# Kernel tuning notes

Measured on AMD Instinct MI355X. Metric: run time of the kernel, lower is better.

The kernel has to match this reference:

```python
import jax, jax.numpy as jnp
import numpy as np

LAMBDA = 0.01  # sparsity_threshold
SCALE = 0.02
NUM_BLOCKS = 4


def setup_inputs() -> dict:
    key = jax.random.key(0)
    k1, k2, k3, k4, k5 = jax.random.split(key, 5)
    B, N, C = 8, 4096, 512
    bs = C // NUM_BLOCKS
    return {
        "x": jax.random.normal(k1, (B, N, C), dtype=jnp.float32),
        "w1": jax.random.normal(k2, (2, NUM_BLOCKS, bs, bs), dtype=jnp.float32) * SCALE,
        "w2": jax.random.normal(k3, (2, NUM_BLOCKS, bs, bs), dtype=jnp.float32) * SCALE,
        "b1": jax.random.normal(k4, (2, NUM_BLOCKS, bs), dtype=jnp.float32) * SCALE,
        "b2": jax.random.normal(k5, (2, NUM_BLOCKS, bs), dtype=jnp.float32) * SCALE,
        "H": 64,
        "W": 64,
    }


def _softshrink(v):
    return jnp.where(v > LAMBDA, v - LAMBDA, jnp.where(v < -LAMBDA, v + LAMBDA, jnp.zeros((), v.dtype)))


def reference(x, w1, w2, b1, b2, H, W):
    B, N, C = x.shape
    bs = C // NUM_BLOCKS
    xb = x.reshape(B, N, NUM_BLOCKS, bs)
    # FFT over (token, block) axes, ortho norm — faithful to torch fft2(dim=(1,2))
    xf = jnp.fft.fft2(xb, axes=(1, 2), norm="ortho")
    re, im = jnp.real(xf), jnp.imag(xf)

    mul = lambda a, w: jnp.einsum("tnbd,bdk->tnbk", a, w)  # block-diagonal matmul

    r1 = jax.nn.relu(mul(re, w1[0]) - mul(im, w1[1]) + b1[0])
    i1 = jax.nn.relu(mul(re, w1[1]) + mul(im, w1[0]) + b1[1])
    r2 = mul(r1, w2[0]) - mul(i1, w2[1]) + b2[0]
    i2 = mul(r1, w2[1]) + mul(i1, w2[0]) + b2[1]

    z = _softshrink(r2) + 1j * _softshrink(i2)
    out = jnp.real(jnp.fft.ifft2(z, axes=(1, 2), norm="ortho"))  # .to(float32) keeps real part
    return out.reshape(B, N, C).astype(jnp.float32)
```

## Files before the change

kernel.cpp:

```cpp
#include <hip/hip_runtime.h>
#include <math.h>

#define TWO_PI 6.283185307179586f

typedef __attribute__((ext_vector_type(8))) short bf16x8;
typedef __attribute__((ext_vector_type(4))) short bf16x4;
typedef __attribute__((ext_vector_type(4))) float f32x4;
typedef __attribute__((ext_vector_type(4))) _Float16 h16x4;
typedef __attribute__((ext_vector_type(8))) _Float16 h16x8;

__device__ __forceinline__ short f2bf(float f) {
    unsigned u = __float_as_uint(f);
    unsigned r = (u + 0x7FFFu + ((u >> 16) & 1u)) >> 16;
    return (short)r;
}
__device__ __forceinline__ float bf2f(short s) {
    return __uint_as_float(((unsigned)(unsigned short)s) << 16);
}

__device__ __forceinline__ int dr4(int s) {
    return ((s & 3) << 4) | (s & 12) | ((s >> 4) & 3);
}

__device__ __forceinline__ void cmulw(float& xr, float& xi, float wr, float wi) {
    const float tr = xr * wr - xi * wi;
    xi = xr * wi + xi * wr;
    xr = tr;
}

template<int W>
__device__ __forceinline__ void fft64_dif4v(_Float16 (*Lre)[W], _Float16 (*Lim)[W],
                                            const float* wtr, const float* wti,
                                            int c4, int h) {
#pragma unroll
    for (int s = 0; s < 3; ++s) {
        const int q  = 16 >> (2 * s);
        const int tw = 1 << (2 * s);
        __syncthreads();
        const int j = h & (q - 1);
        const int g = (s == 0) ? 0 : (h >> (4 - 2 * s));
        const int i0 = g * (q << 2) + j;
        const int i1 = i0 + q, i2 = i1 + q, i3 = i2 + q;
        const h16x4 A0r = *(const h16x4*)&Lre[i0][c4], A0i = *(const h16x4*)&Lim[i0][c4];
        const h16x4 A1r = *(const h16x4*)&Lre[i1][c4], A1i = *(const h16x4*)&Lim[i1][c4];
        const h16x4 A2r = *(const h16x4*)&Lre[i2][c4], A2i = *(const h16x4*)&Lim[i2][c4];
        const h16x4 A3r = *(const h16x4*)&Lre[i3][c4], A3i = *(const h16x4*)&Lim[i3][c4];
        const int m = j * tw;
        const float w1r = wtr[m],     w1i = wti[m];
        const float w2r = wtr[2 * m], w2i = wti[2 * m];
        const float w3r = wtr[3 * m], w3i = wti[3 * m];
        h16x4 O0r, O0i, O1r, O1i, O2r, O2i, O3r, O3i;
#pragma unroll
        for (int e = 0; e < 4; ++e) {
            const float a0r = (float)A0r[e], a0i = (float)A0i[e];
            const float a1r = (float)A1r[e], a1i = (float)A1i[e];
            const float a2r = (float)A2r[e], a2i = (float)A2i[e];
            const float a3r = (float)A3r[e], a3i = (float)A3i[e];
            const float t0r = a0r + a2r, t0i = a0i + a2i;
            const float t2r = a0r - a2r, t2i = a0i - a2i;
            const float t1r = a1r + a3r, t1i = a1i + a3i;
            const float dr  = a1r - a3r, di  = a1i - a3i;
            const float t3r = di, t3i = -dr;
            O0r[e] = (_Float16)(t0r + t1r);  O0i[e] = (_Float16)(t0i + t1i);
            float y1r = t2r + t3r, y1i = t2i + t3i;
            float y2r = t0r - t1r, y2i = t0i - t1i;
            float y3r = t2r - t3r, y3i = t2i - t3i;
            if (m) {
                cmulw(y1r, y1i, w1r, w1i);
                cmulw(y2r, y2i, w2r, w2i);
                cmulw(y3r, y3i, w3r, w3i);
            }
            O1r[e] = (_Float16)y1r; O1i[e] = (_Float16)y1i;
            O2r[e] = (_Float16)y2r; O2i[e] = (_Float16)y2i;
            O3r[e] = (_Float16)y3r; O3i[e] = (_Float16)y3i;
        }
        *(h16x4*)&Lre[i0][c4] = O0r;  *(h16x4*)&Lim[i0][c4] = O0i;
        *(h16x4*)&Lre[i1][c4] = O1r;  *(h16x4*)&Lim[i1][c4] = O1i;
        *(h16x4*)&Lre[i2][c4] = O2r;  *(h16x4*)&Lim[i2][c4] = O2i;
        *(h16x4*)&Lre[i3][c4] = O3r;  *(h16x4*)&Lim[i3][c4] = O3i;
    }
    __syncthreads();
}

template<int W>
__device__ __forceinline__ void fft64_dit4v(_Float16 (*Lre)[W], _Float16 (*Lim)[W],
                                            const float* wtr, const float* wti,
                                            int c4, int h) {
#pragma unroll
    for (int s = 2; s >= 0; --s) {
        const int q  = 16 >> (2 * s);
        const int tw = 1 << (2 * s);
        __syncthreads();
        const int j = h & (q - 1);
        const int g = (s == 0) ? 0 : (h >> (4 - 2 * s));
        const int i0 = g * (q << 2) + j;
        const int i1 = i0 + q, i2 = i1 + q, i3 = i2 + q;
        const h16x4 A0r = *(const h16x4*)&Lre[i0][c4], A0i = *(const h16x4*)&Lim[i0][c4];
        const h16x4 A1r = *(const h16x4*)&Lre[i1][c4], A1i = *(const h16x4*)&Lim[i1][c4];
        const h16x4 A2r = *(const h16x4*)&Lre[i2][c4], A2i = *(const h16x4*)&Lim[i2][c4];
        const h16x4 A3r = *(const h16x4*)&Lre[i3][c4], A3i = *(const h16x4*)&Lim[i3][c4];
        const int m = j * tw;
        const float w1r = wtr[m],     w1i = -wti[m];
        const float w2r = wtr[2 * m], w2i = -wti[2 * m];
        const float w3r = wtr[3 * m], w3i = -wti[3 * m];
        h16x4 O0r, O0i, O1r, O1i, O2r, O2i, O3r, O3i;
#pragma unroll
        for (int e = 0; e < 4; ++e) {
            float b1r = (float)A1r[e], b1i = (float)A1i[e];
            float b2r = (float)A2r[e], b2i = (float)A2i[e];
            float b3r = (float)A3r[e], b3i = (float)A3i[e];
            if (m) {
                cmulw(b1r, b1i, w1r, w1i);
                cmulw(b2r, b2i, w2r, w2i);
                cmulw(b3r, b3i, w3r, w3i);
            }
            const float a0r = (float)A0r[e], a0i = (float)A0i[e];
            const float u0r = a0r + b2r, u0i = a0i + b2i;
            const float u1r = a0r - b2r, u1i = a0i - b2i;
            const float u2r = b1r + b3r, u2i = b1i + b3i;
            const float dr  = b1r - b3r, di  = b1i - b3i;
            const float u3r = -di, u3i = dr;
            O0r[e] = (_Float16)(u0r + u2r); O0i[e] = (_Float16)(u0i + u2i);
            O1r[e] = (_Float16)(u1r + u3r); O1i[e] = (_Float16)(u1i + u3i);
            O2r[e] = (_Float16)(u0r - u2r); O2i[e] = (_Float16)(u0i - u2i);
            O3r[e] = (_Float16)(u1r - u3r); O3i[e] = (_Float16)(u1i - u3i);
        }
        *(h16x4*)&Lre[i0][c4] = O0r;  *(h16x4*)&Lim[i0][c4] = O0i;
        *(h16x4*)&Lre[i1][c4] = O1r;  *(h16x4*)&Lim[i1][c4] = O1i;
        *(h16x4*)&Lre[i2][c4] = O2r;  *(h16x4*)&Lim[i2][c4] = O2i;
        *(h16x4*)&Lre[i3][c4] = O3r;  *(h16x4*)&Lim[i3][c4] = O3i;
    }
    __syncthreads();
}

#define DECODE_BCT() \
    const int b  = blockIdx.x >> 8; \
    const int dg = (blockIdx.x >> 2) & 63; \
    const int ct = blockIdx.x & 3;

#define GADDR(slot, blk, f4) \
    (((size_t)(b * 4096 + (slot)) * 512) + (size_t)((blk) * 128 + ct * 32 + (f4) * 4))

#define GADDR8(slot, blk, e8) \
    (((size_t)(b * 4096 + (slot)) * 512) + (size_t)((blk) * 128 + ct * 32 + (e8) * 8))

#define SETUP_TABLE48() \
    if (tid < 48) { \
        float s_, c_; \
        sincosf(TWO_PI * (float)tid / 64.0f, &s_, &c_); \
        wre[tid] = c_; wim[tid] = -s_; \
    }

extern "C" __global__ void __launch_bounds__(512)
fft_fwd_a(const float* __restrict__ x, short* __restrict__ zre, short* __restrict__ zim) {
    __shared__ __align__(16) _Float16 Lre[64][136];
    __shared__ __align__(16) _Float16 Lim[64][136];
    __shared__ float wre[48], wim[48];
    __shared__ float twr[64], twi[64];
    const int tid = threadIdx.x;
    SETUP_TABLE48();
    DECODE_BCT();
    if (tid >= 64 && tid < 128) {
        const int s1 = tid - 64;
        float sn, cs;
        sincosf(-(TWO_PI / 4096.0f) * (float)(dg * dr4(s1)), &sn, &cs);
        twr[s1] = cs; twi[s1] = sn;
    }
    for (int idx = tid; idx < 2048; idx += 512) {
        const int n1 = idx >> 5, q = idx & 31, blk = q >> 3, f4 = q & 7;
        const int cl = blk * 32 + f4 * 4;
        const float4 v = *(const float4*)(x + GADDR(n1 * 64 + dg, blk, f4));
        h16x4 hv, hz;
        hv[0] = (_Float16)v.x; hv[1] = (_Float16)v.y;
        hv[2] = (_Float16)v.z; hv[3] = (_Float16)v.w;
        hz[0] = (_Float16)0.f; hz[1] = (_Float16)0.f;
        hz[2] = (_Float16)0.f; hz[3] = (_Float16)0.f;
        *(h16x4*)&Lre[n1][cl] = hv;
        *(h16x4*)&Lim[n1][cl] = hz;
    }
    fft64_dif4v<136>(Lre, Lim, wre, wim, (tid & 31) * 4, tid >> 5);
    for (int idx = tid; idx < 2048; idx += 512) {
        const int s1 = idx >> 5, q = idx & 31, blk = q >> 3, f4 = q & 7;
        const int cl = blk * 32 + f4 * 4;
        const float cs = twr[s1], sn = twi[s1];
        const h16x4 hr = *(const h16x4*)&Lre[s1][cl];
        const h16x4 hi = *(const h16x4*)&Lim[s1][cl];
        bf16x4 pr, pi;
#pragma unroll
        for (int i = 0; i < 4; ++i) {
            const float vr = (float)hr[i], vi = (float)hi[i];
            pr[i] = f2bf(vr * cs - vi * sn);
            pi[i] = f2bf(vr * sn + vi * cs);
        }
        const size_t g = GADDR(s1 * 64 + dg, blk, f4);
        *(bf16x4*)(zre + g) = pr;
        *(bf16x4*)(zim + g) = pi;
    }
}

extern "C" __global__ void __launch_bounds__(512)
fft_fwd_b(short* __restrict__ zre, short* __restrict__ zim) {
    __shared__ __align__(16) _Float16 Lre[64][136];
    __shared__ __align__(16) _Float16 Lim[64][136];
    __shared__ float wre[48], wim[48];
    const int tid = threadIdx.x;
    SETUP_TABLE48();
    DECODE_BCT();
    for (int idx = tid; idx < 1024; idx += 512) {
        const int n2 = idx >> 4, q = idx & 15, blk = q >> 2, e8 = q & 3;
        const int cl = blk * 32 + e8 * 8;
        const size_t g = GADDR8(dg * 64 + n2, blk, e8);
        const bf16x8 vr = *(const bf16x8*)(zre + g);
        const bf16x8 vi = *(const bf16x8*)(zim + g);
        h16x8 hr, hi;
#pragma unroll
        for (int i = 0; i < 8; ++i) {
            hr[i] = (_Float16)bf2f(vr[i]);
            hi[i] = (_Float16)bf2f(vi[i]);
        }
        *(h16x8*)&Lre[n2][cl] = hr;
        *(h16x8*)&Lim[n2][cl] = hi;
    }
    fft64_dif4v<136>(Lre, Lim, wre, wim, (tid & 31) * 4, tid >> 5);
    {
        const int s = tid >> 3, dq = tid & 7;
        const int cb = dq * 4;
        h16x4 R[4], M[4];
#pragma unroll
        for (int qq = 0; qq < 4; ++qq) {
            R[qq] = *(const h16x4*)&Lre[s][cb + qq * 32];
            M[qq] = *(const h16x4*)&Lim[s][cb + qq * 32];
        }
        h16x4 YR[4], YM[4];
        const float sc = 1.0f / 128.0f;
#pragma unroll
        for (int e = 0; e < 4; ++e) {
            const float r0 = (float)R[0][e], r1 = (float)R[1][e];
            const float r2 = (float)R[2][e], r3 = (float)R[3][e];
            const float m0 = (float)M[0][e], m1 = (float)M[1][e];
            const float m2 = (float)M[2][e], m3 = (float)M[3][e];
            YR[0][e] = (_Float16)((r0 + r1 + r2 + r3) * sc);
            YM[0][e] = (_Float16)((m0 + m1 + m2 + m3) * sc);
            YR[1][e] = (_Float16)((r0 + m1 - r2 - m3) * sc);
            YM[1][e] = (_Float16)((m0 - r1 - m2 + r3) * sc);
            YR[2][e] = (_Float16)((r0 - r1 + r2 - r3) * sc);
            YM[2][e] = (_Float16)((m0 - m1 + m2 - m3) * sc);
            YR[3][e] = (_Float16)((r0 - m1 - r2 + m3) * sc);
            YM[3][e] = (_Float16)((m0 + r1 - m2 - r3) * sc);
        }
#pragma unroll
        for (int qq = 0; qq < 4; ++qq) {
            *(h16x4*)&Lre[s][cb + qq * 32] = YR[qq];
            *(h16x4*)&Lim[s][cb + qq * 32] = YM[qq];
        }
    }
    __syncthreads();
    for (int idx = tid; idx < 1024; idx += 512) {
        const int s2 = idx >> 4, q = idx & 15, blk = q >> 2, e8 = q & 3;
        const int cl = blk * 32 + e8 * 8;
        const h16x8 hr = *(const h16x8*)&Lre[s2][cl];
        const h16x8 hi = *(const h16x8*)&Lim[s2][cl];
        bf16x8 pr, pi;
#pragma unroll
        for (int i = 0; i < 8; ++i) {
            pr[i] = f2bf((float)hr[i]);
            pi[i] = f2bf((float)hi[i]);
        }
        const size_t g = GADDR8(dg * 64 + s2, blk, e8);
        *(bf16x8*)(zre + g) = pr;
        *(bf16x8*)(zim + g) = pi;
    }
}

extern "C" __global__ void __launch_bounds__(512)
fft_inv_a(short* __restrict__ zre, short* __restrict__ zim) {
    __shared__ __align__(16) _Float16 Lre[64][136];
    __shared__ __align__(16) _Float16 Lim[64][136];
    __shared__ float wre[48], wim[48];
    __shared__ float twr[64], twi[64];
    const int tid = threadIdx.x;
    SETUP_TABLE48();
    DECODE_BCT();
    if (tid >= 64 && tid < 128) {
        const int n2 = tid - 64;
        float sn, cs;
        sincosf((TWO_PI / 4096.0f) * (float)(n2 * dr4(dg)), &sn, &cs);
        twr[n2] = cs; twi[n2] = sn;
    }
    for (int idx = tid; idx < 1024; idx += 512) {
        const int s2 = idx >> 4, q = idx & 15, blk = q >> 2, e8 = q & 3;
        const int cl = blk * 32 + e8 * 8;
        const size_t g = GADDR8(dg * 64 + s2, blk, e8);
        const bf16x8 vr = *(const bf16x8*)(zre + g);
        const bf16x8 vi = *(const bf16x8*)(zim + g);
        h16x8 hr, hi;
#pragma unroll
        for (int i = 0; i < 8; ++i) {
            hr[i] = (_Float16)bf2f(vr[i]);
            hi[i] = (_Float16)bf2f(vi[i]);
        }
        *(h16x8*)&Lre[s2][cl] = hr;
        *(h16x8*)&Lim[s2][cl] = hi;
    }
    __syncthreads();
    {
        const int s = tid >> 3, dq = tid & 7;
        const int cb = dq * 4;
        h16x4 R[4], M[4];
#pragma unroll
        for (int qq = 0; qq < 4; ++qq) {
            R[qq] = *(const h16x4*)&Lre[s][cb + qq * 32];
            M[qq] = *(const h16x4*)&Lim[s][cb + qq * 32];
        }
        h16x4 YR[4], YM[4];
        const float sc = 1.0f / 128.0f;
#pragma unroll
        for (int e = 0; e < 4; ++e) {
            const float r0 = (float)R[0][e], r1 = (float)R[1][e];
            const float r2 = (float)R[2][e], r3 = (float)R[3][e];
            const float m0 = (float)M[0][e], m1 = (float)M[1][e];
            const float m2 = (float)M[2][e], m3 = (float)M[3][e];
            YR[0][e] = (_Float16)((r0 + r1 + r2 + r3) * sc);
            YM[0][e] = (_Float16)((m0 + m1 + m2 + m3) * sc);
            YR[1][e] = (_Float16)((r0 - m1 - r2 + m3) * sc);
            YM[1][e] = (_Float16)((m0 + r1 - m2 - r3) * sc);
            YR[2][e] = (_Float16)((r0 - r1 + r2 - r3) * sc);
            YM[2][e] = (_Float16)((m0 - m1 + m2 - m3) * sc);
            YR[3][e] = (_Float16)((r0 + m1 - r2 - m3) * sc);
            YM[3][e] = (_Float16)((m0 - r1 - m2 + r3) * sc);
        }
#pragma unroll
        for (int qq = 0; qq < 4; ++qq) {
            *(h16x4*)&Lre[s][cb + qq * 32] = YR[qq];
            *(h16x4*)&Lim[s][cb + qq * 32] = YM[qq];
        }
    }
    fft64_dit4v<136>(Lre, Lim, wre, wim, (tid & 31) * 4, tid >> 5);
    for (int idx = tid; idx < 2048; idx += 512) {
        const int n2 = idx >> 5, q = idx & 31, blk = q >> 3, f4 = q & 7;
        const int cl = blk * 32 + f4 * 4;
        const float cs = twr[n2], sn = twi[n2];
        const h16x4 hr = *(const h16x4*)&Lre[n2][cl];
        const h16x4 hi = *(const h16x4*)&Lim[n2][cl];
        bf16x4 pr, pi;
#pragma unroll
        for (int i = 0; i < 4; ++i) {
            const float vr = (float)hr[i], vi = (float)hi[i];
            pr[i] = f2bf(vr * cs - vi * sn);
            pi[i] = f2bf(vr * sn + vi * cs);
        }
        const size_t g = GADDR(dg * 64 + n2, blk, f4);
        *(bf16x4*)(zre + g) = pr;
        *(bf16x4*)(zim + g) = pi;
    }
}

extern "C" __global__ void __launch_bounds__(512)
fft_inv_b(const short* __restrict__ zre, const short* __restrict__ zim,
          float* __restrict__ out) {
    __shared__ __align__(16) _Float16 Lre[64][136];
    __shared__ __align__(16) _Float16 Lim[64][136];
    __shared__ float wre[48], wim[48];
    const int tid = threadIdx.x;
    SETUP_TABLE48();
    DECODE_BCT();
    for (int idx = tid; idx < 1024; idx += 512) {
        const int s1 = idx >> 4, q = idx & 15, blk = q >> 2, e8 = q & 3;
        const int cl = blk * 32 + e8 * 8;
        const size_t g = GADDR8(s1 * 64 + dg, blk, e8);
        const bf16x8 vr = *(const bf16x8*)(zre + g);
        const bf16x8 vi = *(const bf16x8*)(zim + g);
        h16x8 hr, hi;
#pragma unroll
        for (int i = 0; i < 8; ++i) {
            hr[i] = (_Float16)bf2f(vr[i]);
            hi[i] = (_Float16)bf2f(vi[i]);
        }
        *(h16x8*)&Lre[s1][cl] = hr;
        *(h16x8*)&Lim[s1][cl] = hi;
    }
    fft64_dit4v<136>(Lre, Lim, wre, wim, (tid & 31) * 4, tid >> 5);
    for (int idx = tid; idx < 2048; idx += 512) {
        const int n1 = idx >> 5, q = idx & 31, blk = q >> 3, f4 = q & 7;
        const int cl = blk * 32 + f4 * 4;
        const h16x4 hr = *(const h16x4*)&Lre[n1][cl];
        float4 o;
        o.x = (float)hr[0]; o.y = (float)hr[1];
        o.z = (float)hr[2]; o.w = (float)hr[3];
        *(float4*)(out + GADDR(n1 * 64 + dg, blk, f4)) = o;
    }
}

extern "C" __global__ void __launch_bounds__(256)
wprep(const float* __restrict__ w1, const float* __restrict__ w2,
      short* __restrict__ wb) {
    const int i4  = blockIdx.x * 256 + threadIdx.x;
    const int k0  = (i4 & 63) * 4;
    const int n   = (i4 >> 6) & 255;
    const int blk = (i4 >> 14) & 3;
    const int L   = i4 >> 16;
    const float* w = L ? w2 : w1;
    bf16x4 pv;
#pragma unroll
    for (int j = 0; j < 4; ++j) {
        const int k = k0 + j;
        float v;
        if (k < 128) {
            v = (n < 128) ? w[blk * 16384 + k * 128 + n]
                          : w[65536 + blk * 16384 + k * 128 + (n - 128)];
        } else {
            v = (n < 128) ? -w[65536 + blk * 16384 + (k - 128) * 128 + n]
                          :  w[blk * 16384 + (k - 128) * 128 + (n - 128)];
        }
        pv[j] = f2bf(v);
    }
    *(bf16x4*)(wb + (size_t)i4 * 4) = pv;
}

#define MITER 4

__device__ __forceinline__ void stage_tile(const short* __restrict__ zre,
                                           const short* __restrict__ zim,
                                           char* Abuf, int rowbase, int blk,
                                           int wave, int lane) {
#pragma unroll
    for (int it = 0; it < 4; ++it) {
        const int chunk = wave * 256 + it * 64 + lane;
        const int row   = chunk >> 5;
        const unsigned kbyte = ((unsigned)((chunk & 31) << 4)) ^ ((unsigned)((row & 7) << 4));
        const int k0 = (int)(kbyte >> 1);
        const short* src = (k0 < 128) ? zre : zim;
        const size_t g = (size_t)(rowbase + row) * 512 + blk * 128 + (k0 & 127);
        unsigned* lp = (unsigned*)(Abuf + (wave * 4096 + it * 1024));
        __builtin_amdgcn_global_load_lds((const unsigned*)(src + g), lp, 16, 0, 0);
    }
}

template<int LAYER>
__global__ void __launch_bounds__(512)
mlp_mfma(short* __restrict__ zre, short* __restrict__ zim,
         const short* __restrict__ wb, const float* __restrict__ bias) {
    __shared__ __align__(16) char As[2][64 * 256 * 2];

    const int blk  = blockIdx.y;
    const int tid  = threadIdx.x;
    const int wave = tid >> 6;
    const int lane = tid & 63;
    const int lrow = lane & 15;
    const int lk   = lane >> 4;

    bf16x8 Bf[2][8];
#pragma unroll
    for (int nt = 0; nt < 2; ++nt) {
        const int n = wave * 32 + nt * 16 + lrow;
#pragma unroll
        for (int ks = 0; ks < 8; ++ks) {
            Bf[nt][ks] = *(const bf16x8*)(wb + ((size_t)(blk * 256 + n) * 256 + ks * 32 + lk * 8));
        }
    }

    float bv[2];
#pragma unroll
    for (int nt = 0; nt < 2; ++nt) {
        const int n = wave * 32 + nt * 16 + lrow;
        bv[nt] = (n < 128) ? bias[blk * 128 + n] : bias[512 + blk * 128 + (n - 128)];
    }

    stage_tile(zre, zim, As[0], blockIdx.x * MITER * 64, blk, wave, lane);

    for (int t = 0; t < MITER; ++t) {
        __syncthreads();

        if (t + 1 < MITER)
            stage_tile(zre, zim, As[(t + 1) & 1],
                       (blockIdx.x * MITER + t + 1) * 64, blk, wave, lane);

        const char* Ab = As[t & 1];
        const int rowbase = (blockIdx.x * MITER + t) * 64;

        f32x4 acc[4][2];
#pragma unroll
        for (int mt = 0; mt < 4; ++mt)
#pragma unroll
            for (int nt = 0; nt < 2; ++nt)
                acc[mt][nt] = (f32x4){0.f, 0.f, 0.f, 0.f};

#pragma unroll
        for (int ks = 0; ks < 8; ++ks) {
            bf16x8 af[4];
#pragma unroll
            for (int mt = 0; mt < 4; ++mt) {
                const int row = mt * 16 + lrow;
                const int k0  = ks * 32 + lk * 8;
                const unsigned byteoff =
                    ((unsigned)(row * 512 + k0 * 2)) ^ ((unsigned)((row & 7) << 4));
                af[mt] = *(const bf16x8*)(Ab + byteoff);
            }
#pragma unroll
            for (int mt = 0; mt < 4; ++mt)
#pragma unroll
                for (int nt = 0; nt < 2; ++nt)
                    acc[mt][nt] = __builtin_amdgcn_mfma_f32_16x16x32_bf16(
                        af[mt], Bf[nt][ks], acc[mt][nt], 0, 0, 0);
        }

#pragma unroll
        for (int nt = 0; nt < 2; ++nt) {
            const int n = wave * 32 + nt * 16 + lrow;
            short* dst = (n < 128) ? zre : zim;
            const int col = blk * 128 + (n & 127);
#pragma unroll
            for (int mt = 0; mt < 4; ++mt) {
#pragma unroll
                for (int r = 0; r < 4; ++r) {
                    const int row = rowbase + mt * 16 + lk * 4 + r;
                    float v = acc[mt][nt][r] + bv[nt];
                    if (LAYER == 1) {
                        v = fmaxf(v, 0.0f);
                    } else {
                        v = (v > 0.01f) ? v - 0.01f : ((v < -0.01f) ? v + 0.01f : 0.0f);
                    }
                    dst[(size_t)row * 512 + col] = f2bf(v);
                }
            }
        }
    }
}

extern "C" void kernel_launch(void* const* d_in, const int* in_sizes, int n_in,
                              void* d_out, int out_size, void* d_ws, size_t ws_size,
                              hipStream_t stream) {
    const float* x  = (const float*)d_in[0];
    const float* w1 = (const float*)d_in[1];
    const float* w2 = (const float*)d_in[2];
    const float* b1 = (const float*)d_in[3];
    const float* b2 = (const float*)d_in[4];

    float* out = (float*)d_out;
    short* zre = (short*)d_ws;
    short* zim = zre + 16777216;
    short* wb  = (short*)d_out;
    const size_t WB_L = 4ull * 256 * 256;

    wprep<<<512, 256, 0, stream>>>(w1, w2, wb);

    fft_fwd_a<<<2048, 512, 0, stream>>>(x, zre, zim);
    fft_fwd_b<<<2048, 512, 0, stream>>>(zre, zim);

    mlp_mfma<1><<<dim3(32768 / (64 * MITER), 4), 512, 0, stream>>>(zre, zim, wb, b1);
    mlp_mfma<2><<<dim3(32768 / (64 * MITER), 4), 512, 0, stream>>>(zre, zim, wb + WB_L, b2);

    fft_inv_a<<<2048, 512, 0, stream>>>(zre, zim);
    fft_inv_b<<<2048, 512, 0, stream>>>(zre, zim, out);
}
```

Baseline: 221.3 us.

## Move 4-point block-axis DFT from middle FFT kernels into outer kernels

```diff
diff --git a/kernel.cpp b/kernel.cpp
--- a/kernel.cpp
+++ b/kernel.cpp
@@ -179,22 +179,45 @@
         *(h16x4*)&Lim[n1][cl] = hz;
     }
     fft64_dif4v<136>(Lre, Lim, wre, wim, (tid & 31) * 4, tid >> 5);
-    for (int idx = tid; idx < 2048; idx += 512) {
-        const int s1 = idx >> 5, q = idx & 31, blk = q >> 3, f4 = q & 7;
-        const int cl = blk * 32 + f4 * 4;
+    {
+        const int s1 = tid >> 3, f4 = tid & 7;
         const float cs = twr[s1], sn = twi[s1];
-        const h16x4 hr = *(const h16x4*)&Lre[s1][cl];
-        const h16x4 hi = *(const h16x4*)&Lim[s1][cl];
-        bf16x4 pr, pi;
-#pragma unroll
-        for (int i = 0; i < 4; ++i) {
-            const float vr = (float)hr[i], vi = (float)hi[i];
-            pr[i] = f2bf(vr * cs - vi * sn);
-            pi[i] = f2bf(vr * sn + vi * cs);
-        }
-        const size_t g = GADDR(s1 * 64 + dg, blk, f4);
-        *(bf16x4*)(zre + g) = pr;
-        *(bf16x4*)(zim + g) = pi;
+        f32x4 r[4], m[4];
+#pragma unroll
+        for (int blk = 0; blk < 4; ++blk) {
+            const int cl = blk * 32 + f4 * 4;
+            const h16x4 hr = *(const h16x4*)&Lre[s1][cl];
+            const h16x4 hi = *(const h16x4*)&Lim[s1][cl];
+#pragma unroll
+            for (int e = 0; e < 4; ++e) {
+                const float vr = (float)hr[e], vi = (float)hi[e];
+                r[blk][e] = vr * cs - vi * sn;
+                m[blk][e] = vr * sn + vi * cs;
+            }
+        }
+        const float sc = 1.0f / 128.0f;
+        f32x4 yr[4], ym[4];
+#pragma unroll
+        for (int e = 0; e < 4; ++e) {
+            const float r0 = r[0][e], r1 = r[1][e], r2 = r[2][e], r3 = r[3][e];
+            const float m0 = m[0][e], m1 = m[1][e], m2 = m[2][e], m3 = m[3][e];
+            yr[0][e] = (r0 + r1 + r2 + r3) * sc;  ym[0][e] = (m0 + m1 + m2 + m3) * sc;
+            yr[1][e] = (r0 + m1 - r2 - m3) * sc;  ym[1][e] = (m0 - r1 - m2 + r3) * sc;
+            yr[2][e] = (r0 - r1 + r2 - r3) * sc;  ym[2][e] = (m0 - m1 + m2 - m3) * sc;
+            yr[3][e] = (r0 - m1 - r2 + m3) * sc;  ym[3][e] = (m0 + r1 - m2 - r3) * sc;
+        }
+#pragma unroll
+        for (int blk = 0; blk < 4; ++blk) {
+            bf16x4 pr, pi;
+#pragma unroll
+            for (int e = 0; e < 4; ++e) {
+                pr[e] = f2bf(yr[blk][e]);
+                pi[e] = f2bf(ym[blk][e]);
+            }
+            const size_t g = GADDR(s1 * 64 + dg, blk, f4);
+            *(bf16x4*)(zre + g) = pr;
+            *(bf16x4*)(zim + g) = pi;
+        }
     }
 }
 
@@ -222,39 +245,6 @@
         *(h16x8*)&Lim[n2][cl] = hi;
     }
     fft64_dif4v<136>(Lre, Lim, wre, wim, (tid & 31) * 4, tid >> 5);
-    {
-        const int s = tid >> 3, dq = tid & 7;
-        const int cb = dq * 4;
-        h16x4 R[4], M[4];
-#pragma unroll
-        for (int qq = 0; qq < 4; ++qq) {
-            R[qq] = *(const h16x4*)&Lre[s][cb + qq * 32];
-            M[qq] = *(const h16x4*)&Lim[s][cb + qq * 32];
-        }
-        h16x4 YR[4], YM[4];
-        const float sc = 1.0f / 128.0f;
-#pragma unroll
-        for (int e = 0; e < 4; ++e) {
-            const float r0 = (float)R[0][e], r1 = (float)R[1][e];
-            const float r2 = (float)R[2][e], r3 = (float)R[3][e];
-            const float m0 = (float)M[0][e], m1 = (float)M[1][e];
-            const float m2 = (float)M[2][e], m3 = (float)M[3][e];
-            YR[0][e] = (_Float16)((r0 + r1 + r2 + r3) * sc);
-            YM[0][e] = (_Float16)((m0 + m1 + m2 + m3) * sc);
-            YR[1][e] = (_Float16)((r0 + m1 - r2 - m3) * sc);
-            YM[1][e] = (_Float16)((m0 - r1 - m2 + r3) * sc);
-            YR[2][e] = (_Float16)((r0 - r1 + r2 - r3) * sc);
-            YM[2][e] = (_Float16)((m0 - m1 + m2 - m3) * sc);
-            YR[3][e] = (_Float16)((r0 - m1 - r2 + m3) * sc);
-            YM[3][e] = (_Float16)((m0 + r1 - m2 - r3) * sc);
-        }
-#pragma unroll
-        for (int qq = 0; qq < 4; ++qq) {
-            *(h16x4*)&Lre[s][cb + qq * 32] = YR[qq];
-            *(h16x4*)&Lim[s][cb + qq * 32] = YM[qq];
-        }
-    }
-    __syncthreads();
     for (int idx = tid; idx < 1024; idx += 512) {
         const int s2 = idx >> 4, q = idx & 15, blk = q >> 2, e8 = q & 3;
         const int cl = blk * 32 + e8 * 8;
@@ -302,39 +292,6 @@
         *(h16x8*)&Lre[s2][cl] = hr;
         *(h16x8*)&Lim[s2][cl] = hi;
     }
-    __syncthreads();
-    {
-        const int s = tid >> 3, dq = tid & 7;
-        const int cb = dq * 4;
-        h16x4 R[4], M[4];
-#pragma unroll
-        for (int qq = 0; qq < 4; ++qq) {
-            R[qq] = *(const h16x4*)&Lre[s][cb + qq * 32];
-            M[qq] = *(const h16x4*)&Lim[s][cb + qq * 32];
-        }
-        h16x4 YR[4], YM[4];
-        const float sc = 1.0f / 128.0f;
-#pragma unroll
-        for (int e = 0; e < 4; ++e) {
-            const float r0 = (float)R[0][e], r1 = (float)R[1][e];
-            const float r2 = (float)R[2][e], r3 = (float)R[3][e];
-            const float m0 = (float)M[0][e], m1 = (float)M[1][e];
-            const float m2 = (float)M[2][e], m3 = (float)M[3][e];
-            YR[0][e] = (_Float16)((r0 + r1 + r2 + r3) * sc);
-            YM[0][e] = (_Float16)((m0 + m1 + m2 + m3) * sc);
-            YR[1][e] = (_Float16)((r0 - m1 - r2 + m3) * sc);
-            YM[1][e] = (_Float16)((m0 + r1 - m2 - r3) * sc);
-            YR[2][e] = (_Float16)((r0 - r1 + r2 - r3) * sc);
-            YM[2][e] = (_Float16)((m0 - m1 + m2 - m3) * sc);
-            YR[3][e] = (_Float16)((r0 + m1 - r2 - m3) * sc);
-            YM[3][e] = (_Float16)((m0 - r1 - m2 + r3) * sc);
-        }
-#pragma unroll
-        for (int qq = 0; qq < 4; ++qq) {
-            *(h16x4*)&Lre[s][cb + qq * 32] = YR[qq];
-            *(h16x4*)&Lim[s][cb + qq * 32] = YM[qq];
-        }
-    }
     fft64_dit4v<136>(Lre, Lim, wre, wim, (tid & 31) * 4, tid >> 5);
     for (int idx = tid; idx < 2048; idx += 512) {
         const int n2 = idx >> 5, q = idx & 31, blk = q >> 3, f4 = q & 7;
@@ -364,20 +321,43 @@
     const int tid = threadIdx.x;
     SETUP_TABLE48();
     DECODE_BCT();
-    for (int idx = tid; idx < 1024; idx += 512) {
-        const int s1 = idx >> 4, q = idx & 15, blk = q >> 2, e8 = q & 3;
-        const int cl = blk * 32 + e8 * 8;
-        const size_t g = GADDR8(s1 * 64 + dg, blk, e8);
-        const bf16x8 vr = *(const bf16x8*)(zre + g);
-        const bf16x8 vi = *(const bf16x8*)(zim + g);
-        h16x8 hr, hi;
-#pragma unroll
-        for (int i = 0; i < 8; ++i) {
-            hr[i] = (_Float16)bf2f(vr[i]);
-            hi[i] = (_Float16)bf2f(vi[i]);
-        }
-        *(h16x8*)&Lre[s1][cl] = hr;
-        *(h16x8*)&Lim[s1][cl] = hi;
+    {
+        const int s1 = tid >> 3, f4 = tid & 7;
+        f32x4 r[4], m[4];
+#pragma unroll
+        for (int blk = 0; blk < 4; ++blk) {
+            const size_t g = GADDR(s1 * 64 + dg, blk, f4);
+            const bf16x4 vr = *(const bf16x4*)(zre + g);
+            const bf16x4 vi = *(const bf16x4*)(zim + g);
+#pragma unroll
+            for (int e = 0; e < 4; ++e) {
+                r[blk][e] = bf2f(vr[e]);
+                m[blk][e] = bf2f(vi[e]);
+            }
+        }
+        const float sc = 1.0f / 128.0f;
+        f32x4 yr[4], ym[4];
+#pragma unroll
+        for (int e = 0; e < 4; ++e) {
+            const float r0 = r[0][e], r1 = r[1][e], r2 = r[2][e], r3 = r[3][e];
+            const float m0 = m[0][e], m1 = m[1][e], m2 = m[2][e], m3 = m[3][e];
+            yr[0][e] = (r0 + r1 + r2 + r3) * sc;  ym[0][e] = (m0 + m1 + m2 + m3) * sc;
+            yr[1][e] = (r0 - m1 - r2 + m3) * sc;  ym[1][e] = (m0 + r1 - m2 - r3) * sc;
+            yr[2][e] = (r0 - r1 + r2 - r3) * sc;  ym[2][e] = (m0 - m1 + m2 - m3) * sc;
+            yr[3][e] = (r0 + m1 - r2 - m3) * sc;  ym[3][e] = (m0 - r1 - m2 + r3) * sc;
+        }
+#pragma unroll
+        for (int blk = 0; blk < 4; ++blk) {
+            const int cl = blk * 32 + f4 * 4;
+            h16x4 hr, hi;
+#pragma unroll
+            for (int e = 0; e < 4; ++e) {
+                hr[e] = (_Float16)yr[blk][e];
+                hi[e] = (_Float16)ym[blk][e];
+            }
+            *(h16x4*)&Lre[s1][cl] = hr;
+            *(h16x4*)&Lim[s1][cl] = hi;
+        }
     }
     fft64_dit4v<136>(Lre, Lim, wre, wim, (tid & 31) * 4, tid >> 5);
     for (int idx = tid; idx < 2048; idx += 512) {
```

Result: no change. 219.0 us (-1.1%).
